# Kernel optimization log

Measured on AMD Instinct MI355X. Metric: run time of the kernel, lower is better.

## Reference

```python
import jax, jax.numpy as jnp
import numpy as np

B, N, F_IN = 32, 512, 64
HEADS = (8, 8)
HIDS = (64, 64)
EDGE_P = 0.05  # graph density
NEG_SLOPE = 0.2
NEG_INF = -1e20


def setup_inputs() -> dict:
    key = jax.random.key(0)
    ks = jax.random.split(key, 8)
    x = jax.random.normal(ks[0], (B, N, F_IN), dtype=jnp.float32)
    adj = (jax.random.uniform(ks[1], (B, N, N)) < EDGE_P).astype(jnp.float32)
    adj = jnp.maximum(adj, adj.transpose(0, 2, 1))  # symmetric adjacency
    # mask = (batch, row): every (b, n) pair gets the masked softmax
    b_idx = jnp.repeat(jnp.arange(B, dtype=jnp.int32), N)   # [B*N]
    r_idx = jnp.tile(jnp.arange(N, dtype=jnp.int32), B)     # [B*N]
    # layer 0: f_in=64 -> f_out=64, H=8 ; layer 1: f_in=64*8=512 -> f_out=64, H=8
    W0 = jax.random.normal(ks[2], (F_IN, HIDS[0]), dtype=jnp.float32) / jnp.sqrt(jnp.float32(F_IN))
    a_src0 = jax.random.normal(ks[3], (HIDS[0], HEADS[0]), dtype=jnp.float32) / jnp.sqrt(jnp.float32(HIDS[0]))
    a_dst0 = jax.random.normal(ks[4], (HIDS[0], HEADS[0]), dtype=jnp.float32) / jnp.sqrt(jnp.float32(HIDS[0]))
    f_in1 = HIDS[0] * HEADS[0]
    W1 = jax.random.normal(ks[5], (f_in1, HIDS[1]), dtype=jnp.float32) / jnp.sqrt(jnp.float32(f_in1))
    a_src1 = jax.random.normal(ks[6], (HIDS[1], HEADS[1]), dtype=jnp.float32) / jnp.sqrt(jnp.float32(HIDS[1]))
    a_dst1 = jax.random.normal(ks[7], (HIDS[1], HEADS[1]), dtype=jnp.float32) / jnp.sqrt(jnp.float32(HIDS[1]))
    return dict(x=x, adj=adj, b_idx=b_idx, r_idx=r_idx,
                W0=W0, a_src0=a_src0, a_dst0=a_dst0,
                W1=W1, a_src1=a_src1, a_dst1=a_dst1)


def _gat_layer(x, adj, b_idx, r_idx, W, a_src, a_dst):
    # x: [B,N,f_in], adj: [B,N,N] (diag already set), W: [f_in,F], a_*: [F,H]
    hp = x @ W                                        # [B,N,F]
    s = jnp.einsum('bnf,fh->bhn', hp, a_src)          # attn_src
    d = jnp.einsum('bnf,fh->bhn', hp, a_dst)          # attn_dst
    attn = s[:, :, :, None] + d[:, :, None, :]        # [B,H,N,N]
    attn = jnp.where(attn >= 0, attn, NEG_SLOPE * attn)  # leaky_relu(0.2)
    attn = jnp.where(adj[:, None, :, :] == 0, 0.0, attn)  # masked_fill(adj==0, 0)
    rows = attn[b_idx, :, r_idx, :]                   # [K,H,N]
    rows = jnp.where(rows == 0.0, NEG_INF, rows)
    rows = jax.nn.softmax(rows, axis=-1)
    attn = attn.at[b_idx, :, r_idx, :].set(rows)
    return jnp.einsum('bhij,bjf->bhif', attn, hp)     # [B,H,N,F]


def reference(x, adj, b_idx, r_idx, W0, a_src0, a_dst0, W1, a_src1, a_dst1):
    Bn, Nn = x.shape[:2]
    # torch mutates adj in place: adj[batch,row,row] = 1 (self loops)
    adj = adj.at[b_idx, r_idx, r_idx].set(1.0)
    o = _gat_layer(x, adj, b_idx, r_idx, W0, a_src0, a_dst0)      # [B,H,N,F0]
    x1 = jax.nn.elu(o.transpose(0, 2, 1, 3).reshape(Bn, Nn, -1))  # [B,N,H*F0]
    o2 = _gat_layer(x1, adj, b_idx, r_idx, W1, a_src1, a_dst1)    # [B,H,N,F1]
    return o2.mean(axis=1)                                        # [B,N,F1]
```

## Files before the change

kernel.cpp:

```cpp
#include <hip/hip_runtime.h>
#include <hip/hip_bf16.h>
#include <math.h>

#define BB 32
#define NN 512

typedef _Float16 f16x8 __attribute__((ext_vector_type(8)));
typedef __fp16  fp16x2 __attribute__((ext_vector_type(2)));
typedef float f32x4 __attribute__((ext_vector_type(4)));

#define MFMA16(a, b, c) __builtin_amdgcn_mfma_f32_16x16x32_f16(a, b, c, 0, 0, 0)

union AF { f16x8 v; unsigned int u[4]; };

__global__ __launch_bounds__(256) void k_wt_prep(
    const float* __restrict__ W0, _Float16* __restrict__ W0T,
    const float* __restrict__ W1, _Float16* __restrict__ W1T)
{
    int id = blockIdx.x * 256 + threadIdx.x;
    const float* W; _Float16* WT; int KT, task;
    if (id < 512) { W = W0; WT = W0T; KT = 64;  task = id; }
    else          { W = W1; WT = W1T; KT = 512; task = id - 512; }
    int n = task & 63, gabs = task >> 6;
    int c = gabs >> 3, g = gabs & 7;
    f16x8 hv;
#pragma unroll
    for (int e = 0; e < 8; ++e)
        hv[e] = (_Float16)W[(size_t)(gabs * 8 + e) * 64 + n];
    *(f16x8*)(WT + (size_t)n * KT + c * 64 + (g ^ (n & 7)) * 8) = hv;
}

__global__ __launch_bounds__(256) void k_maxd(
    const float* __restrict__ dTg, float* __restrict__ maxd)
{
    __shared__ float sm[4];
    int bh = blockIdx.x;
    int t = threadIdx.x, lane = t & 63, w = t >> 6;
    const float* p = dTg + (size_t)bh * NN;
    float m = fmaxf(p[t], p[t + 256]);
#pragma unroll
    for (int off = 32; off; off >>= 1) m = fmaxf(m, __shfl_xor(m, off));
    if (lane == 0) sm[w] = m;
    __syncthreads();
    if (t == 0) maxd[bh] = fmaxf(fmaxf(sm[0], sm[1]), fmaxf(sm[2], sm[3]));
}

static __device__ __forceinline__ void epi_sd_hpt(
    const float* ctile, const float* asd_f, int row0, int t,
    float* __restrict__ s, float* __restrict__ dTg, _Float16* __restrict__ hpT)
{
    int b = row0 >> 9, jb = row0 & 511;
    if (t < 128) {
        int rr = t >> 3, h = t & 7;
        float sv = 0.f, dv = 0.f;
#pragma unroll
        for (int f = 0; f < 64; ++f) {
            float hv = ctile[rr * 66 + f];
            sv = fmaf(hv, asd_f[f * 8 + h], sv);
            dv = fmaf(hv, asd_f[512 + f * 8 + h], dv);
        }
        s[((size_t)b * NN + jb + rr) * 8 + h] = sv;
        dTg[((size_t)b * 8 + h) * NN + jb + rr] = dv;
    } else {
        int t2 = t - 128;
        int f = t2 >> 1, jl = (t2 & 1) * 8;
        f16x8 hv;
#pragma unroll
        for (int e = 0; e < 8; ++e)
            hv[e] = (_Float16)ctile[(jl + e) * 66 + f];
        *(f16x8*)(hpT + ((size_t)b * 64 + f) * NN + jb + jl) = hv;
    }
}

__global__ __launch_bounds__(256) void k_gemm0(
    const float* __restrict__ x, const _Float16* __restrict__ W0T,
    const float* __restrict__ a_src, const float* __restrict__ a_dst,
    float* __restrict__ s, float* __restrict__ dTg, _Float16* __restrict__ hpT)
{
    __shared__ float ctile[16 * 66];
    __shared__ float asd_f[1024];
    int t = threadIdx.x, row0 = blockIdx.x * 16;
    int lane = t & 63, w = t >> 6, cn = lane & 15, rq = lane >> 4;

    ((float4*)asd_f)[t] = (t < 128) ? ((const float4*)a_src)[t]
                                    : ((const float4*)a_dst)[t - 128];
    f32x4 acc;
#pragma unroll
    for (int e = 0; e < 4; ++e) acc[e] = 0.f;
#pragma unroll
    for (int ks = 0; ks < 2; ++ks) {
        const float* xp = x + (size_t)(row0 + cn) * 64 + ks * 32 + rq * 8;
        float4 x0 = *(const float4*)xp, x1 = *(const float4*)(xp + 4);
        f16x8 ah = {(_Float16)x0.x, (_Float16)x0.y, (_Float16)x0.z, (_Float16)x0.w,
                    (_Float16)x1.x, (_Float16)x1.y, (_Float16)x1.z, (_Float16)x1.w};
        int nn = w * 16 + cn;
        f16x8 bh = *(const f16x8*)(W0T + (size_t)nn * 64 + (((ks * 4 + rq) ^ (nn & 7)) * 8));
        acc = MFMA16(ah, bh, acc);
    }
#pragma unroll
    for (int r = 0; r < 4; ++r)
        ctile[(rq * 4 + r) * 66 + w * 16 + cn] = acc[r];
    __syncthreads();
    epi_sd_hpt(ctile, asd_f, row0, t, s, dTg, hpT);
}

template<int MODE>
__global__ __launch_bounds__(256, 4) void k_attn_fused(
    const float* __restrict__ adj, const float* __restrict__ s,
    const float* __restrict__ dTg, const float* __restrict__ maxd,
    const _Float16* __restrict__ hpT,
    const _Float16* __restrict__ W1T,
    const float* __restrict__ a_src, const float* __restrict__ a_dst,
    float* __restrict__ s_out, float* __restrict__ dTg_out,
    _Float16* __restrict__ hpT_out, float* __restrict__ o_f)
{
    __shared__ __align__(16) char smem[32768];
    _Float16* hT = (_Float16*)smem;

    int blk = blockIdx.x;
    int vb = ((blk & 7) << 7) | (blk >> 3);
    int b = vb >> 5, i0 = (vb & 31) << 4;
    int row0 = vb * 16;
    int t = threadIdx.x, lane = t & 63, w = t >> 6;
    int cn = lane & 15, rq = lane >> 4;
    int h0 = 2 * w, h1 = h0 + 1;
    int myrow = i0 + cn;

    float sv0 = s[((size_t)b * NN + myrow) * 8 + h0];
    float sv1 = s[((size_t)b * NN + myrow) * 8 + h1];
    float M0 = fmaxf(sv0 + maxd[b * 8 + h0], 0.f);
    float M1 = fmaxf(sv1 + maxd[b * 8 + h1], 0.f);

    const float* arow = adj + ((size_t)b * NN + myrow) * NN;
    const float* dg0 = dTg + ((size_t)b * 8 + h0) * NN;
    const float* dg1 = dTg + ((size_t)b * 8 + h1) * NN;
    const _Float16* hb = hpT + (size_t)b * 64 * NN;

    int f0 = t >> 3, g0 = t & 7;
    int f1 = f0 + 32;
    int sw = ((g0 ^ (f0 & 7)) * 8);
    int sw0 = f0 * 64 + sw, sw1 = f1 * 64 + sw;

    f16x8 ones;
#pragma unroll
    for (int e = 0; e < 8; ++e) ones[e] = (_Float16)1.0f;

    f32x4 acc[2][4], accrs[2];
#pragma unroll
    for (int hh = 0; hh < 2; ++hh) {
#pragma unroll
        for (int e = 0; e < 4; ++e) accrs[hh][e] = 0.f;
#pragma unroll
        for (int ft = 0; ft < 4; ++ft)
#pragma unroll
            for (int e = 0; e < 4; ++e) acc[hh][ft][e] = 0.f;
    }

    uint4 rH0 = *(const uint4*)(hb + (size_t)f0 * 512 + g0 * 8);
    uint4 rH1 = *(const uint4*)(hb + (size_t)f1 * 512 + g0 * 8);

    for (int jcx = 0; jcx < 8; ++jcx) {
        int jc = jcx * 64;
        float aa[2][8], dd0[2][8], dd1[2][8];
#pragma unroll
        for (int ks = 0; ks < 2; ++ks) {
            int j0 = jc + ks * 32 + rq * 8;
            *(float4*)&aa[ks][0]  = *(const float4*)(arow + j0);
            *(float4*)&aa[ks][4]  = *(const float4*)(arow + j0 + 4);
            *(float4*)&dd0[ks][0] = *(const float4*)(dg0 + j0);
            *(float4*)&dd0[ks][4] = *(const float4*)(dg0 + j0 + 4);
            *(float4*)&dd1[ks][0] = *(const float4*)(dg1 + j0);
            *(float4*)&dd1[ks][4] = *(const float4*)(dg1 + j0 + 4);
        }
        *(uint4*)&hT[sw0] = rH0;
        *(uint4*)&hT[sw1] = rH1;
        __syncthreads();
        if (jcx < 7) {
            rH0 = *(const uint4*)(hb + (size_t)f0 * 512 + jc + 64 + g0 * 8);
            rH1 = *(const uint4*)(hb + (size_t)f1 * 512 + jc + 64 + g0 * 8);
        }
#pragma unroll
        for (int ks = 0; ks < 2; ++ks) {
            int j0 = jc + ks * 32 + rq * 8;
            int rel = myrow - j0;
            AF aA, aB;
#pragma unroll
            for (int e = 0; e < 8; e += 2) {
                float pA[2], pB[2];
#pragma unroll
                for (int q = 0; q < 2; ++q) {
                    int ee = e + q;
                    bool con = (aa[ks][ee] != 0.f) || (ee == rel);
                    float e0 = sv0 + dd0[ks][ee];
                    float l0 = fmaxf(e0, 0.2f * e0);
                    float p0 = __expf(l0 - M0);
                    pA[q] = (con && l0 != 0.f) ? p0 : 0.f;
                    float e1 = sv1 + dd1[ks][ee];
                    float l1 = fmaxf(e1, 0.2f * e1);
                    float p1 = __expf(l1 - M1);
                    pB[q] = (con && l1 != 0.f) ? p1 : 0.f;
                }
                fp16x2 ka = __builtin_amdgcn_cvt_pkrtz(pA[0], pA[1]);
                fp16x2 kb = __builtin_amdgcn_cvt_pkrtz(pB[0], pB[1]);
                aA.u[e >> 1] = __builtin_bit_cast(unsigned int, ka);
                aB.u[e >> 1] = __builtin_bit_cast(unsigned int, kb);
            }
            accrs[0] = MFMA16(aA.v, ones, accrs[0]);
            accrs[1] = MFMA16(aB.v, ones, accrs[1]);
#pragma unroll
            for (int ft = 0; ft < 4; ++ft) {
                int f = ft * 16 + cn;
                f16x8 bh = *(const f16x8*)&hT[f * 64 + (((ks * 4 + rq) ^ (f & 7)) * 8)];
                acc[0][ft] = MFMA16(aA.v, bh, acc[0][ft]);
                acc[1][ft] = MFMA16(aB.v, bh, acc[1][ft]);
            }
        }
        __syncthreads();
    }

    float invr[2][4];
#pragma unroll
    for (int hh = 0; hh < 2; ++hh)
#pragma unroll
        for (int r = 0; r < 4; ++r) invr[hh][r] = 1.0f / accrs[hh][r];

    if (MODE == 0) {
        _Float16* x1all = (_Float16*)(smem + 8192);
#pragma unroll
        for (int hh = 0; hh < 2; ++hh) {
            int h = h0 + hh;
#pragma unroll
            for (int ft = 0; ft < 4; ++ft)
#pragma unroll
                for (int r = 0; r < 4; ++r) {
                    int il = rq * 4 + r;
                    float v = acc[hh][ft][r] * invr[hh][r];
                    v = v > 0.f ? v : __expf(v) - 1.f;
                    int f = ft * 16 + cn;
                    x1all[h * 1024 + il * 64 + (((f >> 3) ^ (il & 7)) * 8) + (f & 7)] =
                        (_Float16)v;
                }
        }

        _Float16* Bst[2] = { (_Float16*)smem, (_Float16*)(smem + 24576) };
        {
#pragma unroll
            for (int u = 0; u < 2; ++u) {
                int idx = t + u * 256;
                *(uint4*)&Bst[0][idx * 8] =
                    *(const uint4*)(W1T + (size_t)(idx >> 3) * 512 + (idx & 7) * 8);
            }
        }
        f32x4 g1;
#pragma unroll
        for (int e = 0; e < 4; ++e) g1[e] = 0.f;
        uint4 rB0, rB1;
        for (int kc = 0; kc < 8; ++kc) {
            int cur = kc & 1;
            if (kc < 7) {
                rB0 = *(const uint4*)(W1T + (size_t)(t >> 3) * 512 + (kc + 1) * 64 + (t & 7) * 8);
                rB1 = *(const uint4*)(W1T + (size_t)((t + 256) >> 3) * 512 + (kc + 1) * 64 + (t & 7) * 8);
            }
            __syncthreads();
#pragma unroll
            for (int ks = 0; ks < 2; ++ks) {
                int pa = (((ks * 4 + rq) ^ (cn & 7)) * 8);
                f16x8 ah = *(const f16x8*)&x1all[kc * 1024 + cn * 64 + pa];
                int nn = w * 16 + cn;
                f16x8 bh = *(const f16x8*)&Bst[cur][nn * 64 + (((ks * 4 + rq) ^ (nn & 7)) * 8)];
                g1 = MFMA16(ah, bh, g1);
            }
            if (kc < 7) {
                *(uint4*)&Bst[cur ^ 1][t * 8] = rB0;
                *(uint4*)&Bst[cur ^ 1][(t + 256) * 8] = rB1;
            }
        }
        __syncthreads();
        float* ctile = (float*)(smem + 8192);
        float* asd_f = (float*)(smem + 16384);
#pragma unroll
        for (int r = 0; r < 4; ++r)
            ctile[(rq * 4 + r) * 66 + w * 16 + cn] = g1[r];
        ((float4*)asd_f)[t] = (t < 128) ? ((const float4*)a_src)[t]
                                        : ((const float4*)a_dst)[t - 128];
        __syncthreads();
        epi_sd_hpt(ctile, asd_f, row0, t, s_out, dTg_out, hpT_out);
    } else {
        float* red = (float*)smem;
#pragma unroll
        for (int ft = 0; ft < 4; ++ft)
#pragma unroll
            for (int r = 0; r < 4; ++r) {
                int il = rq * 4 + r;
                float v = acc[0][ft][r] * invr[0][r]
                        + acc[1][ft][r] * invr[1][r];
                red[(w * 16 + il) * 64 + ft * 16 + cn] = v;
            }
        __syncthreads();
#pragma unroll
        for (int u = 0; u < 4; ++u) {
            int idx = t + u * 256;
            int il = idx >> 6, f = idx & 63;
            float sum = red[il * 64 + f] + red[(16 + il) * 64 + f]
                      + red[(32 + il) * 64 + f] + red[(48 + il) * 64 + f];
            o_f[((size_t)b * NN + i0 + il) * 64 + f] = sum * 0.125f;
        }
    }
}

extern "C" void kernel_launch(void* const* d_in, const int* in_sizes, int n_in,
                              void* d_out, int out_size, void* d_ws, size_t ws_size,
                              hipStream_t stream) {
    const float* x      = (const float*)d_in[0];
    const float* adj    = (const float*)d_in[1];
    const float* W0     = (const float*)d_in[4];
    const float* a_src0 = (const float*)d_in[5];
    const float* a_dst0 = (const float*)d_in[6];
    const float* W1     = (const float*)d_in[7];
    const float* a_src1 = (const float*)d_in[8];
    const float* a_dst1 = (const float*)d_in[9];
    float* out = (float*)d_out;

    float* ws = (float*)d_ws;
    const size_t R = (size_t)BB * NN;
    float* s0    = ws;
    float* dTg0  = s0 + R * 8;
    float* s1    = dTg0 + (size_t)BB * 8 * NN;
    float* dTg1  = s1 + R * 8;
    float* maxd0 = dTg1 + (size_t)BB * 8 * NN;
    float* maxd1 = maxd0 + 256;
    _Float16* hp0T = (_Float16*)(maxd1 + 256);
    _Float16* hp1T = hp0T + (size_t)BB * 64 * NN;
    _Float16* W0T  = hp1T + (size_t)BB * 64 * NN;
    _Float16* W1T  = W0T + (size_t)64 * 64;

    k_wt_prep<<<18, 256, 0, stream>>>(W0, W0T, W1, W1T);
    k_gemm0<<<1024, 256, 0, stream>>>(x, W0T, a_src0, a_dst0, s0, dTg0, hp0T);
    k_maxd<<<256, 256, 0, stream>>>(dTg0, maxd0);
    k_attn_fused<0><<<1024, 256, 0, stream>>>(adj, s0, dTg0, maxd0, hp0T,
                                              W1T, a_src1, a_dst1,
                                              s1, dTg1, hp1T, nullptr);
    k_maxd<<<256, 256, 0, stream>>>(dTg1, maxd1);
    k_attn_fused<1><<<1024, 256, 0, stream>>>(adj, s1, dTg1, maxd1, hp1T,
                                              nullptr, nullptr, nullptr,
                                              nullptr, nullptr, nullptr, out);
}
```

Before: 165.1 us.

## Fuse max-reduction into epilogue via atomics and double-buffer attention loop loads

Removes the two k_maxd launches by computing per-(batch,head) max of dst scores in the GEMM epilogues with order-preserving float encoding and atomicMax, zeroed in the weight-prep kernel. In the attention kernel, the hp tile is now double-buffered in shared memory and the adjacency/dst loads for the next chunk are prefetched into registers during the current chunk's compute, so only one barrier per iteration is needed. Shared memory offsets for later phases are remapped to fit. The changes add atomic contention and extra register pressure at 4 blocks per CU.

```diff
diff --git a/kernel.cpp b/kernel.cpp
--- a/kernel.cpp
+++ b/kernel.cpp
@@ -13,11 +13,22 @@
 
 union AF { f16x8 v; unsigned int u[4]; };
 
+static __device__ __forceinline__ unsigned int fenc(float x) {
+    unsigned int u = __float_as_uint(x);
+    return (u & 0x80000000u) ? ~u : (u | 0x80000000u);
+}
+static __device__ __forceinline__ float fdec(unsigned int k) {
+    unsigned int u = (k & 0x80000000u) ? (k ^ 0x80000000u) : ~k;
+    return __uint_as_float(u);
+}
+
 __global__ __launch_bounds__(256) void k_wt_prep(
     const float* __restrict__ W0, _Float16* __restrict__ W0T,
-    const float* __restrict__ W1, _Float16* __restrict__ W1T)
+    const float* __restrict__ W1, _Float16* __restrict__ W1T,
+    unsigned int* __restrict__ maxdK)
 {
     int id = blockIdx.x * 256 + threadIdx.x;
+    if (id < 512) maxdK[id] = 0u;
     const float* W; _Float16* WT; int KT, task;
     if (id < 512) { W = W0; WT = W0T; KT = 64;  task = id; }
     else          { W = W1; WT = W1T; KT = 512; task = id - 512; }
@@ -30,24 +41,10 @@
     *(f16x8*)(WT + (size_t)n * KT + c * 64 + (g ^ (n & 7)) * 8) = hv;
 }
 
-__global__ __launch_bounds__(256) void k_maxd(
-    const float* __restrict__ dTg, float* __restrict__ maxd)
-{
-    __shared__ float sm[4];
-    int bh = blockIdx.x;
-    int t = threadIdx.x, lane = t & 63, w = t >> 6;
-    const float* p = dTg + (size_t)bh * NN;
-    float m = fmaxf(p[t], p[t + 256]);
-#pragma unroll
-    for (int off = 32; off; off >>= 1) m = fmaxf(m, __shfl_xor(m, off));
-    if (lane == 0) sm[w] = m;
-    __syncthreads();
-    if (t == 0) maxd[bh] = fmaxf(fmaxf(sm[0], sm[1]), fmaxf(sm[2], sm[3]));
-}
-
 static __device__ __forceinline__ void epi_sd_hpt(
     const float* ctile, const float* asd_f, int row0, int t,
-    float* __restrict__ s, float* __restrict__ dTg, _Float16* __restrict__ hpT)
+    float* __restrict__ s, float* __restrict__ dTg, _Float16* __restrict__ hpT,
+    unsigned int* __restrict__ maxdK)
 {
     int b = row0 >> 9, jb = row0 & 511;
     if (t < 128) {
@@ -61,6 +58,11 @@
         }
         s[((size_t)b * NN + jb + rr) * 8 + h] = sv;
         dTg[((size_t)b * 8 + h) * NN + jb + rr] = dv;
+        float m = dv;
+        m = fmaxf(m, __shfl_xor(m, 8));
+        m = fmaxf(m, __shfl_xor(m, 16));
+        m = fmaxf(m, __shfl_xor(m, 32));
+        if ((t & 63) < 8) atomicMax(maxdK + b * 8 + h, fenc(m));
     } else {
         int t2 = t - 128;
         int f = t2 >> 1, jl = (t2 & 1) * 8;
@@ -75,7 +77,8 @@
 __global__ __launch_bounds__(256) void k_gemm0(
     const float* __restrict__ x, const _Float16* __restrict__ W0T,
     const float* __restrict__ a_src, const float* __restrict__ a_dst,
-    float* __restrict__ s, float* __restrict__ dTg, _Float16* __restrict__ hpT)
+    float* __restrict__ s, float* __restrict__ dTg, _Float16* __restrict__ hpT,
+    unsigned int* __restrict__ maxdK)
 {
     __shared__ float ctile[16 * 66];
     __shared__ float asd_f[1024];
@@ -101,21 +104,21 @@
     for (int r = 0; r < 4; ++r)
         ctile[(rq * 4 + r) * 66 + w * 16 + cn] = acc[r];
     __syncthreads();
-    epi_sd_hpt(ctile, asd_f, row0, t, s, dTg, hpT);
+    epi_sd_hpt(ctile, asd_f, row0, t, s, dTg, hpT, maxdK);
 }
 
 template<int MODE>
 __global__ __launch_bounds__(256, 4) void k_attn_fused(
     const float* __restrict__ adj, const float* __restrict__ s,
-    const float* __restrict__ dTg, const float* __restrict__ maxd,
+    const float* __restrict__ dTg, const unsigned int* __restrict__ maxdK,
     const _Float16* __restrict__ hpT,
     const _Float16* __restrict__ W1T,
     const float* __restrict__ a_src, const float* __restrict__ a_dst,
     float* __restrict__ s_out, float* __restrict__ dTg_out,
-    _Float16* __restrict__ hpT_out, float* __restrict__ o_f)
+    _Float16* __restrict__ hpT_out, unsigned int* __restrict__ maxdK_out,
+    float* __restrict__ o_f)
 {
     __shared__ __align__(16) char smem[32768];
-    _Float16* hT = (_Float16*)smem;
 
     int blk = blockIdx.x;
     int vb = ((blk & 7) << 7) | (blk >> 3);
@@ -128,8 +131,8 @@
 
     float sv0 = s[((size_t)b * NN + myrow) * 8 + h0];
     float sv1 = s[((size_t)b * NN + myrow) * 8 + h1];
-    float M0 = fmaxf(sv0 + maxd[b * 8 + h0], 0.f);
-    float M1 = fmaxf(sv1 + maxd[b * 8 + h1], 0.f);
+    float M0 = fmaxf(sv0 + fdec(maxdK[b * 8 + h0]), 0.f);
+    float M1 = fmaxf(sv1 + fdec(maxdK[b * 8 + h1]), 0.f);
 
     const float* arow = adj + ((size_t)b * NN + myrow) * NN;
     const float* dg0 = dTg + ((size_t)b * 8 + h0) * NN;
@@ -158,32 +161,36 @@
 
     uint4 rH0 = *(const uint4*)(hb + (size_t)f0 * 512 + g0 * 8);
     uint4 rH1 = *(const uint4*)(hb + (size_t)f1 * 512 + g0 * 8);
+    float aa[2][8], dd0[2][8], dd1[2][8];
+#pragma unroll
+    for (int ks = 0; ks < 2; ++ks) {
+        int j0 = ks * 32 + rq * 8;
+        *(float4*)&aa[ks][0]  = *(const float4*)(arow + j0);
+        *(float4*)&aa[ks][4]  = *(const float4*)(arow + j0 + 4);
+        *(float4*)&dd0[ks][0] = *(const float4*)(dg0 + j0);
+        *(float4*)&dd0[ks][4] = *(const float4*)(dg0 + j0 + 4);
+        *(float4*)&dd1[ks][0] = *(const float4*)(dg1 + j0);
+        *(float4*)&dd1[ks][4] = *(const float4*)(dg1 + j0 + 4);
+    }
+    {
+        _Float16* hT0 = (_Float16*)smem;
+        *(uint4*)&hT0[sw0] = rH0;
+        *(uint4*)&hT0[sw1] = rH1;
+    }
+    __syncthreads();
+    rH0 = *(const uint4*)(hb + (size_t)f0 * 512 + 64 + g0 * 8);
+    rH1 = *(const uint4*)(hb + (size_t)f1 * 512 + 64 + g0 * 8);
 
     for (int jcx = 0; jcx < 8; ++jcx) {
         int jc = jcx * 64;
-        float aa[2][8], dd0[2][8], dd1[2][8];
-#pragma unroll
-        for (int ks = 0; ks < 2; ++ks) {
-            int j0 = jc + ks * 32 + rq * 8;
-            *(float4*)&aa[ks][0]  = *(const float4*)(arow + j0);
-            *(float4*)&aa[ks][4]  = *(const float4*)(arow + j0 + 4);
-            *(float4*)&dd0[ks][0] = *(const float4*)(dg0 + j0);
-            *(float4*)&dd0[ks][4] = *(const float4*)(dg0 + j0 + 4);
-            *(float4*)&dd1[ks][0] = *(const float4*)(dg1 + j0);
-            *(float4*)&dd1[ks][4] = *(const float4*)(dg1 + j0 + 4);
-        }
-        *(uint4*)&hT[sw0] = rH0;
-        *(uint4*)&hT[sw1] = rH1;
-        __syncthreads();
-        if (jcx < 7) {
-            rH0 = *(const uint4*)(hb + (size_t)f0 * 512 + jc + 64 + g0 * 8);
-            rH1 = *(const uint4*)(hb + (size_t)f1 * 512 + jc + 64 + g0 * 8);
-        }
+        _Float16* hTc = (_Float16*)(smem + (jcx & 1) * 8192);
+        _Float16* hTn = (_Float16*)(smem + ((jcx & 1) ^ 1) * 8192);
+
+        AF aA[2], aB[2];
 #pragma unroll
         for (int ks = 0; ks < 2; ++ks) {
             int j0 = jc + ks * 32 + rq * 8;
             int rel = myrow - j0;
-            AF aA, aB;
 #pragma unroll
             for (int e = 0; e < 8; e += 2) {
                 float pA[2], pB[2];
@@ -202,17 +209,40 @@
                 }
                 fp16x2 ka = __builtin_amdgcn_cvt_pkrtz(pA[0], pA[1]);
                 fp16x2 kb = __builtin_amdgcn_cvt_pkrtz(pB[0], pB[1]);
-                aA.u[e >> 1] = __builtin_bit_cast(unsigned int, ka);
-                aB.u[e >> 1] = __builtin_bit_cast(unsigned int, kb);
-            }
-            accrs[0] = MFMA16(aA.v, ones, accrs[0]);
-            accrs[1] = MFMA16(aB.v, ones, accrs[1]);
+                aA[ks].u[e >> 1] = __builtin_bit_cast(unsigned int, ka);
+                aB[ks].u[e >> 1] = __builtin_bit_cast(unsigned int, kb);
+            }
+        }
+        if (jcx < 7) {
+#pragma unroll
+            for (int ks = 0; ks < 2; ++ks) {
+                int j0 = jc + 64 + ks * 32 + rq * 8;
+                *(float4*)&aa[ks][0]  = *(const float4*)(arow + j0);
+                *(float4*)&aa[ks][4]  = *(const float4*)(arow + j0 + 4);
+                *(float4*)&dd0[ks][0] = *(const float4*)(dg0 + j0);
+                *(float4*)&dd0[ks][4] = *(const float4*)(dg0 + j0 + 4);
+                *(float4*)&dd1[ks][0] = *(const float4*)(dg1 + j0);
+                *(float4*)&dd1[ks][4] = *(const float4*)(dg1 + j0 + 4);
+            }
+        }
+#pragma unroll
+        for (int ks = 0; ks < 2; ++ks) {
+            accrs[0] = MFMA16(aA[ks].v, ones, accrs[0]);
+            accrs[1] = MFMA16(aB[ks].v, ones, accrs[1]);
 #pragma unroll
             for (int ft = 0; ft < 4; ++ft) {
                 int f = ft * 16 + cn;
-                f16x8 bh = *(const f16x8*)&hT[f * 64 + (((ks * 4 + rq) ^ (f & 7)) * 8)];
-                acc[0][ft] = MFMA16(aA.v, bh, acc[0][ft]);
-                acc[1][ft] = MFMA16(aB.v, bh, acc[1][ft]);
+                f16x8 bh = *(const f16x8*)&hTc[f * 64 + (((ks * 4 + rq) ^ (f & 7)) * 8)];
+                acc[0][ft] = MFMA16(aA[ks].v, bh, acc[0][ft]);
+                acc[1][ft] = MFMA16(aB[ks].v, bh, acc[1][ft]);
+            }
+        }
+        if (jcx < 7) {
+            *(uint4*)&hTn[sw0] = rH0;
+            *(uint4*)&hTn[sw1] = rH1;
+            if (jcx < 6) {
+                rH0 = *(const uint4*)(hb + (size_t)f0 * 512 + jc + 128 + g0 * 8);
+                rH1 = *(const uint4*)(hb + (size_t)f1 * 512 + jc + 128 + g0 * 8);
             }
         }
         __syncthreads();
@@ -225,7 +255,7 @@
         for (int r = 0; r < 4; ++r) invr[hh][r] = 1.0f / accrs[hh][r];
 
     if (MODE == 0) {
-        _Float16* x1all = (_Float16*)(smem + 8192);
+        _Float16* x1all = (_Float16*)smem;
 #pragma unroll
         for (int hh = 0; hh < 2; ++hh) {
             int h = h0 + hh;
@@ -242,7 +272,7 @@
                 }
         }
 
-        _Float16* Bst[2] = { (_Float16*)smem, (_Float16*)(smem + 24576) };
+        _Float16* Bst[2] = { (_Float16*)(smem + 16384), (_Float16*)(smem + 24576) };
         {
 #pragma unroll
             for (int u = 0; u < 2; ++u) {
@@ -276,15 +306,15 @@
             }
         }
         __syncthreads();
-        float* ctile = (float*)(smem + 8192);
-        float* asd_f = (float*)(smem + 16384);
+        float* ctile = (float*)smem;
+        float* asd_f = (float*)(smem + 4352);
 #pragma unroll
         for (int r = 0; r < 4; ++r)
             ctile[(rq * 4 + r) * 66 + w * 16 + cn] = g1[r];
         ((float4*)asd_f)[t] = (t < 128) ? ((const float4*)a_src)[t]
                                         : ((const float4*)a_dst)[t - 128];
         __syncthreads();
-        epi_sd_hpt(ctile, asd_f, row0, t, s_out, dTg_out, hpT_out);
+        epi_sd_hpt(ctile, asd_f, row0, t, s_out, dTg_out, hpT_out, maxdK_out);
     } else {
         float* red = (float*)smem;
 #pragma unroll
@@ -327,21 +357,20 @@
     float* dTg0  = s0 + R * 8;
     float* s1    = dTg0 + (size_t)BB * 8 * NN;
     float* dTg1  = s1 + R * 8;
-    float* maxd0 = dTg1 + (size_t)BB * 8 * NN;
-    float* maxd1 = maxd0 + 256;
-    _Float16* hp0T = (_Float16*)(maxd1 + 256);
+    unsigned int* maxdK = (unsigned int*)(dTg1 + (size_t)BB * 8 * NN);
+    unsigned int* maxd0K = maxdK;
+    unsigned int* maxd1K = maxdK + 256;
+    _Float16* hp0T = (_Float16*)(maxdK + 512);
     _Float16* hp1T = hp0T + (size_t)BB * 64 * NN;
     _Float16* W0T  = hp1T + (size_t)BB * 64 * NN;
     _Float16* W1T  = W0T + (size_t)64 * 64;
 
-    k_wt_prep<<<18, 256, 0, stream>>>(W0, W0T, W1, W1T);
-    k_gemm0<<<1024, 256, 0, stream>>>(x, W0T, a_src0, a_dst0, s0, dTg0, hp0T);
-    k_maxd<<<256, 256, 0, stream>>>(dTg0, maxd0);
-    k_attn_fused<0><<<1024, 256, 0, stream>>>(adj, s0, dTg0, maxd0, hp0T,
+    k_wt_prep<<<18, 256, 0, stream>>>(W0, W0T, W1, W1T, maxdK);
+    k_gemm0<<<1024, 256, 0, stream>>>(x, W0T, a_src0, a_dst0, s0, dTg0, hp0T, maxd0K);
+    k_attn_fused<0><<<1024, 256, 0, stream>>>(adj, s0, dTg0, maxd0K, hp0T,
                                               W1T, a_src1, a_dst1,
-                                              s1, dTg1, hp1T, nullptr);
-    k_maxd<<<256, 256, 0, stream>>>(dTg1, maxd1);
-    k_attn_fused<1><<<1024, 256, 0, stream>>>(adj, s1, dTg1, maxd1, hp1T,
+                                              s1, dTg1, hp1T, maxd1K, nullptr);
+    k_attn_fused<1><<<1024, 256, 0, stream>>>(adj, s1, dTg1, maxd1K, hp1T,
                                               nullptr, nullptr, nullptr,
-                                              nullptr, nullptr, nullptr, out);
-}
+                                              nullptr, nullptr, nullptr, nullptr, out);
+}
```

After: 167.3 us. Within noise of the previous version (+1.3%).
